# Kernel optimization log

Hardware: AMD Instinct MI355X
Metric: run time of the kernel (lower is better)

The kernel has to match this reference:

```python
import jax, jax.numpy as jnp
import numpy as np

V, E, H, L, B, T = 50257, 1024, 16, 8, 2, 2048
HD = E // H  # head_dim = 64
FF = 4 * E
EPS = 1e-5


def setup_inputs() -> dict:
    key = jax.random.key(0)
    ks = jax.random.split(key, 12)
    s = 0.02  # init std as in _init_weights
    return {
        "idx": jax.random.randint(ks[0], (B, T), 0, V, dtype=jnp.int64) if jax.config.jax_enable_x64 else jax.random.randint(ks[0], (B, T), 0, V, dtype=jnp.int32),
        "targets": jax.random.randint(ks[1], (B, T), 0, V, dtype=jnp.int32),
        "wte": jax.random.normal(ks[2], (V, E), jnp.float32) * s,
        "wpe": jax.random.normal(ks[3], (T, E), jnp.float32) * s,
        "qkv_w": jax.random.normal(ks[4], (L, E, 3 * E), jnp.float32) * s,
        "proj_w": jax.random.normal(ks[5], (L, E, E), jnp.float32) * s,
        "proj_b": jnp.zeros((L, E), jnp.float32),
        "ln1_g": jnp.ones((L, E), jnp.float32),
        "ln1_b": jnp.zeros((L, E), jnp.float32),
        "ln2_g": jnp.ones((L, E), jnp.float32),
        "ln2_b": jnp.zeros((L, E), jnp.float32),
        "fc1_w": jax.random.normal(ks[6], (L, E, FF), jnp.float32) * s,
        "fc1_b": jnp.zeros((L, FF), jnp.float32),
        "fc2_w": jax.random.normal(ks[7], (L, FF, E), jnp.float32) * s,
        "fc2_b": jnp.zeros((L, E), jnp.float32),
        "lnf_g": jnp.ones((E,), jnp.float32),
        "lnf_b": jnp.zeros((E,), jnp.float32),
    }


def _layer_norm(x, g, b):
    mean = x.mean(-1, keepdims=True)
    var = ((x - mean) ** 2).mean(-1, keepdims=True)  # unbiased=False
    return g * (x - mean) / jnp.sqrt(var + EPS) + b


def _gpt_forward(idx, targets, wte, wpe, qkv_w, proj_w, proj_b,
                 ln1_g, ln1_b, ln2_g, ln2_b, fc1_w, fc1_b, fc2_w, fc2_b,
                 lnf_g, lnf_b):
    Bq, Tq = idx.shape
    x = wte[idx] + wpe[:Tq][None, :, :]  # [B,T,E]
    causal = jnp.tril(jnp.ones((Tq, Tq), bool))  # [T,T]
    scale = 1.0 / np.sqrt(HD)

    def block(x, p):
        (qw, pw, pb, g1, b1, g2, b2, f1w, f1b, f2w, f2b) = p
        h = _layer_norm(x, g1, b1)
        qkv = h @ qw  # [B,T,3E]
        qkv = qkv.reshape(Bq, Tq, 3, H, HD).transpose(2, 0, 3, 1, 4)  # [3,B,H,T,HD]
        q, k, v = qkv[0], qkv[1], qkv[2]
        att = jnp.einsum('bhqd,bhkd->bhqk', q, k) * scale
        att = jnp.where(causal[None, None], att, -jnp.inf)
        att = jax.nn.softmax(att, axis=-1)  # dropout=0.0 -> identity
        y = jnp.einsum('bhqk,bhkd->bhqd', att, v)
        y = y.transpose(0, 2, 1, 3).reshape(Bq, Tq, E)
        x = x + y @ pw + pb
        h = _layer_norm(x, g2, b2)
        h = jax.nn.gelu(h @ f1w + f1b, approximate=False)  # torch nn.GELU = exact erf
        x = x + h @ f2w + f2b
        return x, None

    params = (qkv_w, proj_w, proj_b, ln1_g, ln1_b, ln2_g, ln2_b,
              fc1_w, fc1_b, fc2_w, fc2_b)
    x, _ = jax.lax.scan(block, x, params)
    x = _layer_norm(x, lnf_g, lnf_b)
    logits = x @ wte.T  # tied lm_head, [B,T,V]
    logp = jax.nn.log_softmax(logits, axis=-1)
    nll = -jnp.take_along_axis(logp, targets[..., None], axis=-1)[..., 0]
    loss = nll.mean()
    return logits, loss


def reference(idx, targets, wte, wpe, qkv_w, proj_w, proj_b,
              ln1_g, ln1_b, ln2_g, ln2_b, fc1_w, fc1_b, fc2_w, fc2_b,
              lnf_g, lnf_b):
    return _gpt_forward(idx, targets, wte, wpe, qkv_w, proj_w, proj_b,
                        ln1_g, ln1_b, ln2_g, ln2_b, fc1_w, fc1_b, fc2_w, fc2_b,
                        lnf_g, lnf_b)
```

## Files before the change

kernel.cpp:

```cpp
#include <hip/hip_runtime.h>
#include <math.h>

constexpr int Vv = 50257;
constexpr int Ee = 1024;
constexpr int Hh = 16;
constexpr int Ll = 8;
constexpr int Bb = 2;
constexpr int Tt = 2048;
constexpr int HDh = 64;
constexpr int FFf = 4096;
constexpr int BT = Bb * Tt;

typedef __attribute__((ext_vector_type(8))) short bf16x8;
typedef __attribute__((ext_vector_type(4))) float f32x4;

__device__ __forceinline__ short f2b(float f) {
    union { float f; unsigned u; } c; c.f = f;
    unsigned u = c.u + 0x7fffu + ((c.u >> 16) & 1u);
    return (short)(u >> 16);
}

__device__ __forceinline__ void g2l16(void* lds, const void* g) {
    __builtin_amdgcn_global_load_lds(
        (const __attribute__((address_space(1))) void*)g,
        (__attribute__((address_space(3))) void*)lds, 16, 0, 0);
}

__device__ __forceinline__ float gelu_exact(float v) {
    return 0.5f * v * (1.0f + erff(v * 0.70710678118654752f));
}

__global__ __launch_bounds__(256) void k_embed(const int* __restrict__ idx,
                                               const float* __restrict__ wte,
                                               const float* __restrict__ wpe,
                                               float* __restrict__ x) {
    const int row = blockIdx.x;
    const int t = row % Tt;
    const int tok = idx[row];
    const int c = threadIdx.x * 4;
    const float4 a = *(const float4*)(wte + (size_t)tok * Ee + c);
    const float4 b = *(const float4*)(wpe + (size_t)t * Ee + c);
    *(float4*)(x + (size_t)row * Ee + c) =
        make_float4(a.x + b.x, a.y + b.y, a.z + b.z, a.w + b.w);
}

__global__ __launch_bounds__(256) void k_ln(const float* __restrict__ x,
                                            const float* __restrict__ g,
                                            const float* __restrict__ b,
                                            short* __restrict__ out) {
    const int row = blockIdx.x;
    const int tid = threadIdx.x;
    const float4 v = *(const float4*)(x + (size_t)row * Ee + tid * 4);
    float s  = v.x + v.y + v.z + v.w;
    float ss = v.x * v.x + v.y * v.y + v.z * v.z + v.w * v.w;
#pragma unroll
    for (int off = 32; off; off >>= 1) {
        s  += __shfl_down(s, off);
        ss += __shfl_down(ss, off);
    }
    __shared__ float red[8];
    const int wid = tid >> 6, lane = tid & 63;
    if (lane == 0) { red[wid] = s; red[4 + wid] = ss; }
    __syncthreads();
    const float S  = red[0] + red[1] + red[2] + red[3];
    const float SS = red[4] + red[5] + red[6] + red[7];
    const float mean = S * (1.f / Ee);
    const float var  = SS * (1.f / Ee) - mean * mean;
    const float inv  = rsqrtf(var + 1e-5f);
    const float4 gg = *(const float4*)(g + tid * 4);
    const float4 bb = *(const float4*)(b + tid * 4);
    short4 o;
    o.x = f2b((v.x - mean) * inv * gg.x + bb.x);
    o.y = f2b((v.y - mean) * inv * gg.y + bb.y);
    o.z = f2b((v.z - mean) * inv * gg.z + bb.z);
    o.w = f2b((v.w - mean) * inv * gg.w + bb.w);
    *(short4*)(out + (size_t)row * Ee + tid * 4) = o;
}

__global__ __launch_bounds__(256) void k_wT(const float* __restrict__ w,
                                            short* __restrict__ o, int K, int N) {
    __shared__ short t[32][33];
    const int n0 = blockIdx.x * 32, k0 = blockIdx.y * 32;
    const int tid = threadIdx.x;
    {
        const int k = tid >> 3, n4 = (tid & 7) * 4;
        const float4 v = *(const float4*)(w + (size_t)(k0 + k) * N + n0 + n4);
        t[n4 + 0][k] = f2b(v.x); t[n4 + 1][k] = f2b(v.y);
        t[n4 + 2][k] = f2b(v.z); t[n4 + 3][k] = f2b(v.w);
    }
    __syncthreads();
    {
        const int n = tid >> 3, k4 = (tid & 7) * 4;
        short4 s;
        s.x = t[n][k4]; s.y = t[n][k4 + 1]; s.z = t[n][k4 + 2]; s.w = t[n][k4 + 3];
        *(short4*)(o + (size_t)(n0 + n) * K + k0 + k4) = s;
    }
}

__global__ __launch_bounds__(256) void k_vT(const short* __restrict__ qkv,
                                            short* __restrict__ vT) {
    __shared__ short t[32][33];
    const int r0 = blockIdx.x * 32;
    const int c0 = blockIdx.y * 32;
    const int tid = threadIdx.x;
    {
        const int r = tid >> 3, c4 = (tid & 7) * 4;
        const short4 v = *(const short4*)(qkv + (size_t)(r0 + r) * (3 * Ee) + 2 * Ee + c0 + c4);
        t[c4 + 0][r] = v.x; t[c4 + 1][r] = v.y;
        t[c4 + 2][r] = v.z; t[c4 + 3][r] = v.w;
    }
    __syncthreads();
    {
        const int c = tid >> 3, r4 = (tid & 7) * 4;
        short4 s;
        s.x = t[c][r4]; s.y = t[c][r4 + 1]; s.z = t[c][r4 + 2]; s.w = t[c][r4 + 3];
        *(short4*)(vT + (size_t)(c0 + c) * BT + r0 + r4) = s;
    }
}

__global__ __launch_bounds__(256) void k_cvt(const float* __restrict__ w,
                                             short* __restrict__ o, int n8) {
    const int i = blockIdx.x * 256 + threadIdx.x;
    if (i >= n8) return;
    const float4 a = ((const float4*)w)[i * 2];
    const float4 b = ((const float4*)w)[i * 2 + 1];
    bf16x8 v = {f2b(a.x), f2b(a.y), f2b(a.z), f2b(a.w),
                f2b(b.x), f2b(b.y), f2b(b.z), f2b(b.w)};
    ((bf16x8*)o)[i] = v;
}

__device__ __forceinline__ void st_c(float* C, size_t i, float v) { C[i] = v; }
__device__ __forceinline__ void st_c(short* C, size_t i, float v) { C[i] = f2b(v); }

template <int EPI, int SWZ, int BN64f, int WAVES, typename OT>
__global__ __launch_bounds__(WAVES * 64) void k_gemm(const short* __restrict__ A,
                                              const short* __restrict__ Bp,
                                              const float* __restrict__ bias,
                                              const float* __restrict__ res,
                                              OT* __restrict__ C,
                                              int M, int N, int K,
                                              float* __restrict__ pmax,
                                              float* __restrict__ psum) {
    constexpr int BM = (WAVES / 2) * 64;
    constexpr int BN = BN64f ? 64 : 128;
    constexpr int NJ = BN64f ? 2 : 4;
    constexpr int WCOL = BN64f ? 32 : 64;
    __shared__ short As[2][BM * 32];
    __shared__ short Bs[2][BN * 32];
    const int tid = threadIdx.x, w = tid >> 6, ln = tid & 63;
    int bx = blockIdx.x, by = blockIdx.y;
    if (SWZ) {
        const int nwg = gridDim.x * gridDim.y;
        const int orig = by * gridDim.x + bx;
        const int q = nwg >> 3, r = nwg & 7;
        const int xcd = orig & 7, local = orig >> 3;
        const int wgid = (xcd < r ? xcd * (q + 1) : r * (q + 1) + (xcd - r) * q) + local;
        if (SWZ == 1) { bx = wgid % gridDim.x; by = wgid / gridDim.x; }
        else          { bx = wgid / gridDim.y; by = wgid % gridDim.y; }
    }
    const int m0 = bx * BM, n0 = by * BN;
    const int wr = w >> 1, wc = w & 1;

    f32x4 zero = {0.f, 0.f, 0.f, 0.f};
    f32x4 acc[4][NJ];
#pragma unroll
    for (int i = 0; i < 4; i++)
#pragma unroll
        for (int j = 0; j < NJ; j++) acc[i][j] = zero;

    const int srow = w * 32 + (ln >> 2);
    const int scol = (ln & 3) * 8;
    const int sb   = tid >> 2;
    const int sb8  = w * 16 + (ln >> 2);
    const int br0 = min(n0 + srow, N - 1);
    const int br1 = min(n0 + srow + 16, N - 1);
    const int brs = min(n0 + sb, N - 1);
    const int br8 = min(n0 + sb8, N - 1);

    auto STAGE = [&](int buf, int k0) {
        short* As_ = As[buf];
        short* Bs_ = Bs[buf];
        g2l16(&As_[(w * 32 + 0) * 32],  A + (size_t)(m0 + srow) * K + k0 + scol);
        g2l16(&As_[(w * 32 + 16) * 32], A + (size_t)(m0 + srow + 16) * K + k0 + scol);
        if (BN64f) {
            g2l16(&Bs_[sb * 32], Bp + (size_t)brs * K + k0 + scol);
        } else if (WAVES == 8) {
            g2l16(&Bs_[(w * 16) * 32], Bp + (size_t)br8 * K + k0 + scol);
        } else {
            g2l16(&Bs_[(w * 32 + 0) * 32],  Bp + (size_t)br0 * K + k0 + scol);
            g2l16(&Bs_[(w * 32 + 16) * 32], Bp + (size_t)br1 * K + k0 + scol);
        }
    };

    int cur = 0;
    STAGE(0, 0);
    __syncthreads();
    for (int k0 = 0; k0 < K; k0 += 32) {
        if (k0 + 32 < K) STAGE(cur ^ 1, k0 + 32);
        const short* Ar = As[cur];
        const short* Br = Bs[cur];
        bf16x8 af[4], bfv[NJ];
#pragma unroll
        for (int i = 0; i < 4; i++)
            af[i]  = *(const bf16x8*)&Ar[(wr * 64 + i * 16 + (ln & 15)) * 32 + (ln >> 4) * 8];
#pragma unroll
        for (int j = 0; j < NJ; j++)
            bfv[j] = *(const bf16x8*)&Br[(wc * WCOL + j * 16 + (ln & 15)) * 32 + (ln >> 4) * 8];
#pragma unroll
        for (int i = 0; i < 4; i++)
#pragma unroll
            for (int j = 0; j < NJ; j++)
                acc[i][j] = __builtin_amdgcn_mfma_f32_16x16x32_bf16(
                    af[i], bfv[j], acc[i][j], 0, 0, 0);
        __syncthreads();
        cur ^= 1;
    }

#pragma unroll
    for (int j = 0; j < NJ; j++) {
        const int gcol = n0 + wc * WCOL + j * 16 + (ln & 15);
        if (gcol < N) {
            const float bv = (EPI == 2 || EPI == 3) ? bias[gcol] : 0.f;
#pragma unroll
            for (int i = 0; i < 4; i++) {
#pragma unroll
                for (int r = 0; r < 4; r++) {
                    const int grow = m0 + wr * 64 + i * 16 + (ln >> 4) * 4 + r;
                    float v = acc[i][j][r] + bv;
                    if (EPI == 2) v = gelu_exact(v);
                    if (EPI == 3) v += res[(size_t)grow * N + gcol];
                    st_c(C, (size_t)grow * N + gcol, v);
                }
            }
        }
    }
    if (EPI == 4) {
        const size_t slot = (size_t)(by * 2 + wc) * M;
#pragma unroll
        for (int i = 0; i < 4; i++) {
#pragma unroll
            for (int r = 0; r < 4; r++) {
                const int grow = m0 + wr * 64 + i * 16 + (ln >> 4) * 4 + r;
                float vv[NJ], pm = -INFINITY;
#pragma unroll
                for (int j = 0; j < NJ; j++) {
                    const int gcol = n0 + wc * WCOL + j * 16 + (ln & 15);
                    vv[j] = (gcol < N) ? acc[i][j][r] : -INFINITY;
                    pm = fmaxf(pm, vv[j]);
                }
#pragma unroll
                for (int off = 1; off < 16; off <<= 1) pm = fmaxf(pm, __shfl_xor(pm, off));
                float ps = 0.f;
#pragma unroll
                for (int j = 0; j < NJ; j++)
                    ps += (vv[j] > -INFINITY) ? __expf(vv[j] - pm) : 0.f;
#pragma unroll
                for (int off = 1; off < 16; off <<= 1) ps += __shfl_xor(ps, off);
                if ((ln & 15) == 0) {
                    pmax[slot + grow] = pm;
                    psum[slot + grow] = ps;
                }
            }
        }
    }
}

__global__ __launch_bounds__(256) void k_attn(const short* __restrict__ qkv,
                                              const short* __restrict__ vT,
                                              short* __restrict__ y) {
    __shared__ short Kl[64][72];
    __shared__ short Vt[64][72];
    __shared__ short Pl[4][16][72];
    const int tid = threadIdx.x, w = tid >> 6, ln = tid & 63;
    const int lo = blockIdx.x;
    const int hi = (Tt / 64 - 1) - lo;
    const int h = blockIdx.y, b = blockIdx.z;
    const size_t base = ((size_t)b * Tt) * (3 * Ee) + h * HDh;
    const int q0s[2] = {lo * 64, hi * 64};

    bf16x8 qf[2][2];
#pragma unroll
    for (int s = 0; s < 2; s++) {
        const int qr = q0s[s] + w * 16 + (ln & 15);
        const short* qp = qkv + base + (size_t)qr * (3 * Ee) + (ln >> 4) * 8;
        qf[s][0] = *(const bf16x8*)(qp);
        qf[s][1] = *(const bf16x8*)(qp + 32);
    }

    f32x4 zero = {0.f, 0.f, 0.f, 0.f};
    f32x4 oc[2][4];
#pragma unroll
    for (int s = 0; s < 2; s++)
#pragma unroll
        for (int i = 0; i < 4; i++) oc[s][i] = zero;
    float mx[2][4], ls[2][4];
#pragma unroll
    for (int s = 0; s < 2; s++)
#pragma unroll
        for (int r = 0; r < 4; r++) { mx[s][r] = -INFINITY; ls[s][r] = 0.f; }

    const int nt = hi + 1;
    for (int j = 0; j < nt; j++) {
        const int kb = j * 64;
        __syncthreads();
        {
            const int r = tid >> 2, d0 = (tid & 3) * 16;
            const short* kp = qkv + base + Ee + (size_t)(kb + r) * (3 * Ee) + d0;
            *(bf16x8*)&Kl[r][d0]     = *(const bf16x8*)(kp);
            *(bf16x8*)&Kl[r][d0 + 8] = *(const bf16x8*)(kp + 8);
            const short* vp = vT + (size_t)(h * HDh + r) * BT + (size_t)b * Tt + kb + d0;
            *(bf16x8*)&Vt[r][d0]     = *(const bf16x8*)(vp);
            *(bf16x8*)&Vt[r][d0 + 8] = *(const bf16x8*)(vp + 8);
        }
        __syncthreads();

#pragma unroll
        for (int s = 1; s >= 0; s--) {
            if (s == 0 && j > lo) continue;
            f32x4 sc[4];
#pragma unroll
            for (int kcb = 0; kcb < 4; kcb++) {
                const int krow = kcb * 16 + (ln & 15);
                bf16x8 kf0 = *(bf16x8*)&Kl[krow][(ln >> 4) * 8];
                bf16x8 kf1 = *(bf16x8*)&Kl[krow][(ln >> 4) * 8 + 32];
                f32x4 ss = __builtin_amdgcn_mfma_f32_16x16x32_bf16(qf[s][0], kf0, zero, 0, 0, 0);
                sc[kcb]  = __builtin_amdgcn_mfma_f32_16x16x32_bf16(qf[s][1], kf1, ss, 0, 0, 0);
            }
            float pv[4][4];
            float tmv[4] = {-INFINITY, -INFINITY, -INFINITY, -INFINITY};
#pragma unroll
            for (int kcb = 0; kcb < 4; kcb++) {
                const int col = kb + kcb * 16 + (ln & 15);
#pragma unroll
                for (int r = 0; r < 4; r++) {
                    const int qr = q0s[s] + w * 16 + (ln >> 4) * 4 + r;
                    const float sv = (col <= qr) ? sc[kcb][r] * 0.125f : -INFINITY;
                    pv[kcb][r] = sv;
                    tmv[r] = fmaxf(tmv[r], sv);
                }
            }
#pragma unroll
            for (int off = 1; off < 16; off <<= 1)
#pragma unroll
                for (int r = 0; r < 4; r++) tmv[r] = fmaxf(tmv[r], __shfl_xor(tmv[r], off));
            float rs[4];
#pragma unroll
            for (int r = 0; r < 4; r++) {
                const float nm = fmaxf(mx[s][r], tmv[r]);
                const float alpha = __expf(mx[s][r] - nm);
                mx[s][r] = nm;
                float acc_s = 0.f;
#pragma unroll
                for (int kcb = 0; kcb < 4; kcb++) {
                    const float e = __expf(pv[kcb][r] - nm);
                    pv[kcb][r] = e;
                    acc_s += e;
                }
                rs[r] = acc_s;
                ls[s][r] *= alpha;
#pragma unroll
                for (int db = 0; db < 4; db++) oc[s][db][r] *= alpha;
            }
#pragma unroll
            for (int off = 1; off < 16; off <<= 1)
#pragma unroll
                for (int r = 0; r < 4; r++) rs[r] += __shfl_xor(rs[r], off);
#pragma unroll
            for (int r = 0; r < 4; r++) ls[s][r] += rs[r];
#pragma unroll
            for (int kcb = 0; kcb < 4; kcb++)
#pragma unroll
                for (int r = 0; r < 4; r++)
                    Pl[w][(ln >> 4) * 4 + r][kcb * 16 + (ln & 15)] = f2b(pv[kcb][r]);
            bf16x8 pf0 = *(bf16x8*)&Pl[w][ln & 15][(ln >> 4) * 8];
            bf16x8 pf1 = *(bf16x8*)&Pl[w][ln & 15][(ln >> 4) * 8 + 32];
#pragma unroll
            for (int db = 0; db < 4; db++) {
                const int drow = db * 16 + (ln & 15);
                bf16x8 vf0 = *(bf16x8*)&Vt[drow][(ln >> 4) * 8];
                bf16x8 vf1 = *(bf16x8*)&Vt[drow][(ln >> 4) * 8 + 32];
                oc[s][db] = __builtin_amdgcn_mfma_f32_16x16x32_bf16(pf0, vf0, oc[s][db], 0, 0, 0);
                oc[s][db] = __builtin_amdgcn_mfma_f32_16x16x32_bf16(pf1, vf1, oc[s][db], 0, 0, 0);
            }
        }
    }
#pragma unroll
    for (int s = 0; s < 2; s++)
#pragma unroll
        for (int r = 0; r < 4; r++) {
            const int qr = q0s[s] + w * 16 + (ln >> 4) * 4 + r;
            const float inv = 1.f / ls[s][r];
#pragma unroll
            for (int db = 0; db < 4; db++)
                y[(size_t)(b * Tt + qr) * Ee + h * HDh + db * 16 + (ln & 15)] =
                    f2b(oc[s][db][r] * inv);
        }
}

__global__ __launch_bounds__(256) void k_loss_fin(const float* __restrict__ pmax,
                                                  const float* __restrict__ psum,
                                                  const float* __restrict__ logits,
                                                  const int* __restrict__ targets,
                                                  float* __restrict__ rnll, int nt2) {
    const int row = blockIdx.x * 256 + threadIdx.x;
    float M = -INFINITY, S = 0.f;
    for (int i = 0; i < nt2; i++) {
        const float pm = pmax[(size_t)i * BT + row];
        const float ps = psum[(size_t)i * BT + row];
        const float nm = fmaxf(M, pm);
        S = S * __expf(M - nm) + ps * __expf(pm - nm);
        M = nm;
    }
    rnll[row] = (M + logf(S)) - logits[(size_t)row * Vv + targets[row]];
}

__global__ __launch_bounds__(256) void k_loss_final(const float* __restrict__ rnll,
                                                    float* __restrict__ loss) {
    const int tid = threadIdx.x;
    float s = 0.f;
    for (int i = tid; i < BT; i += 256) s += rnll[i];
#pragma unroll
    for (int off = 32; off; off >>= 1) s += __shfl_xor(s, off);
    __shared__ float red[4];
    if ((tid & 63) == 0) red[tid >> 6] = s;
    __syncthreads();
    if (tid == 0) loss[0] = (red[0] + red[1] + red[2] + red[3]) / (float)BT;
}

extern "C" void kernel_launch(void* const* d_in, const int* in_sizes, int n_in,
                              void* d_out, int out_size, void* d_ws, size_t ws_size,
                              hipStream_t stream) {
    const int*   idx     = (const int*)d_in[0];
    const int*   targets = (const int*)d_in[1];
    const float* wte     = (const float*)d_in[2];
    const float* wpe     = (const float*)d_in[3];
    const float* qkv_w   = (const float*)d_in[4];
    const float* proj_w  = (const float*)d_in[5];
    const float* proj_b  = (const float*)d_in[6];
    const float* ln1_g   = (const float*)d_in[7];
    const float* ln1_b   = (const float*)d_in[8];
    const float* ln2_g   = (const float*)d_in[9];
    const float* ln2_b   = (const float*)d_in[10];
    const float* fc1_w   = (const float*)d_in[11];
    const float* fc1_b   = (const float*)d_in[12];
    const float* fc2_w   = (const float*)d_in[13];
    const float* fc2_b   = (const float*)d_in[14];
    const float* lnf_g   = (const float*)d_in[15];
    const float* lnf_b   = (const float*)d_in[16];

    float* logits = (float*)d_out;
    float* loss   = logits + (size_t)BT * Vv;

    constexpr int NT2 = 2 * ((Vv + 127) / 128);

    short* wteb = (short*)d_ws;
    float* x    = (float*)d_ws;
    short* qkvb = (short*)(x + (size_t)BT * Ee);
    short* y    = qkvb + (size_t)BT * 3 * Ee;
    short* h1   = y + (size_t)BT * Ee;
    short* wT   = h1 + (size_t)BT * FFf;
    short* vT   = wT + (size_t)FFf * Ee;
    const size_t OFF = (size_t)Vv * Ee * 2;
    short* h    = (short*)((char*)d_ws + OFF);
    float* rnll = (float*)(h + (size_t)BT * Ee);
    float* pmax = rnll + BT;
    float* psum = pmax + (size_t)BT * NT2;
    const size_t need = OFF + (size_t)BT * Ee * 2
                      + (BT + 2 * (size_t)BT * NT2) * sizeof(float);
    if (ws_size < need) return;

    k_embed<<<BT, 256, 0, stream>>>(idx, wte, wpe, x);
    for (int l = 0; l < Ll; l++) {
        k_ln<<<BT, 256, 0, stream>>>(x, ln1_g + (size_t)l * Ee, ln1_b + (size_t)l * Ee, h);
        k_wT<<<dim3(3 * Ee / 32, Ee / 32), 256, 0, stream>>>(
            qkv_w + (size_t)l * Ee * 3 * Ee, wT, Ee, 3 * Ee);
        k_gemm<0, 1, 0, 8, short><<<dim3(BT / 256, 3 * Ee / 128), 512, 0, stream>>>(
            h, wT, nullptr, nullptr, qkvb, BT, 3 * Ee, Ee, nullptr, nullptr);
        k_vT<<<dim3(BT / 32, Ee / 32), 256, 0, stream>>>(qkvb, vT);
        k_attn<<<dim3(Tt / 128, Hh, Bb), 256, 0, stream>>>(qkvb, vT, y);
        k_wT<<<dim3(Ee / 32, Ee / 32), 256, 0, stream>>>(
            proj_w + (size_t)l * Ee * Ee, wT, Ee, Ee);
        k_gemm<3, 1, 1, 4, float><<<dim3(BT / 128, Ee / 64), 256, 0, stream>>>(
            y, wT, proj_b + (size_t)l * Ee, x, x, BT, Ee, Ee, nullptr, nullptr);
        k_ln<<<BT, 256, 0, stream>>>(x, ln2_g + (size_t)l * Ee, ln2_b + (size_t)l * Ee, h);
        k_wT<<<dim3(FFf / 32, Ee / 32), 256, 0, stream>>>(
            fc1_w + (size_t)l * Ee * FFf, wT, Ee, FFf);
        k_gemm<2, 1, 0, 8, short><<<dim3(BT / 256, FFf / 128), 512, 0, stream>>>(
            h, wT, fc1_b + (size_t)l * FFf, nullptr, h1, BT, FFf, Ee, nullptr, nullptr);
        k_wT<<<dim3(Ee / 32, FFf / 32), 256, 0, stream>>>(
            fc2_w + (size_t)l * FFf * Ee, wT, FFf, Ee);
        k_gemm<3, 1, 1, 4, float><<<dim3(BT / 128, Ee / 64), 256, 0, stream>>>(
            h1, wT, fc2_b + (size_t)l * Ee, x, x, BT, Ee, FFf, nullptr, nullptr);
    }
    k_ln<<<BT, 256, 0, stream>>>(x, lnf_g, lnf_b, h);
    k_cvt<<<(Vv * Ee / 8 + 255) / 256, 256, 0, stream>>>(wte, wteb, Vv * Ee / 8);
    k_gemm<4, 2, 0, 8, float><<<dim3(BT / 256, (Vv + 127) / 128), 512, 0, stream>>>(
        h, wteb, nullptr, nullptr, logits, BT, Vv, Ee, pmax, psum);
    k_loss_fin<<<BT / 256, 256, 0, stream>>>(pmax, psum, logits, targets, rnll, NT2);
    k_loss_final<<<1, 256, 0, stream>>>(rnll, loss);
}
```

Before: 3.478 ms.

## Fuse layernorm, weight transposes and V transpose into combined prep launches; double-buffer attention K/V

LayerNorm, weight transpose-conversion and V transpose are merged into one multi-role kernel dispatched by block index. This cuts the per-layer launch count and lets the independent pieces run concurrently; a second weight buffer lets fc1 and fc2 weights be prepared together, and vT now reuses the h1 buffer. The attention kernel double-buffers K/V tiles in shared memory, prefetching the next tile into registers while computing the current one, removing one barrier per iteration. The cost is more LDS per attention block and a reworked workspace layout.

Result: no change. 3.449 ms (median of 2 runs) (-0.9%).

```diff
diff --git a/kernel.cpp b/kernel.cpp
--- a/kernel.cpp
+++ b/kernel.cpp
@@ -77,44 +77,80 @@
     *(short4*)(out + (size_t)row * Ee + tid * 4) = o;
 }
 
-__global__ __launch_bounds__(256) void k_wT(const float* __restrict__ w,
-                                            short* __restrict__ o, int K, int N) {
-    __shared__ short t[32][33];
-    const int n0 = blockIdx.x * 32, k0 = blockIdx.y * 32;
-    const int tid = threadIdx.x;
+__global__ __launch_bounds__(256) void k_prep(
+    const float* __restrict__ x, const float* __restrict__ g,
+    const float* __restrict__ b, short* __restrict__ hout, int nln,
+    const float* __restrict__ w1, short* __restrict__ o1, int K1, int N1, int nw1,
+    const float* __restrict__ w2, short* __restrict__ o2, int K2, int N2, int nw2,
+    const short* __restrict__ qkvsrc, short* __restrict__ vTo, int nvt) {
+    __shared__ float red[8];
+    __shared__ short tl[32][33];
+    const int blk = blockIdx.x, tid = threadIdx.x;
+    if (blk < nln) {
+        const int row = blk;
+        const float4 v = *(const float4*)(x + (size_t)row * Ee + tid * 4);
+        float s  = v.x + v.y + v.z + v.w;
+        float ss = v.x * v.x + v.y * v.y + v.z * v.z + v.w * v.w;
+#pragma unroll
+        for (int off = 32; off; off >>= 1) {
+            s  += __shfl_down(s, off);
+            ss += __shfl_down(ss, off);
+        }
+        const int wid = tid >> 6, lane = tid & 63;
+        if (lane == 0) { red[wid] = s; red[4 + wid] = ss; }
+        __syncthreads();
+        const float S  = red[0] + red[1] + red[2] + red[3];
+        const float SS = red[4] + red[5] + red[6] + red[7];
+        const float mean = S * (1.f / Ee);
+        const float var  = SS * (1.f / Ee) - mean * mean;
+        const float inv  = rsqrtf(var + 1e-5f);
+        const float4 gg = *(const float4*)(g + tid * 4);
+        const float4 bb = *(const float4*)(b + tid * 4);
+        short4 o;
+        o.x = f2b((v.x - mean) * inv * gg.x + bb.x);
+        o.y = f2b((v.y - mean) * inv * gg.y + bb.y);
+        o.z = f2b((v.z - mean) * inv * gg.z + bb.z);
+        o.w = f2b((v.w - mean) * inv * gg.w + bb.w);
+        *(short4*)(hout + (size_t)row * Ee + tid * 4) = o;
+        return;
+    }
+    int t = blk - nln;
+    if (t >= nw1 + nw2) {
+        t -= nw1 + nw2;
+        const int rx = BT / 32;
+        const int r0 = (t % rx) * 32, c0 = (t / rx) * 32;
+        {
+            const int r = tid >> 3, c4 = (tid & 7) * 4;
+            const short4 v = *(const short4*)(qkvsrc + (size_t)(r0 + r) * (3 * Ee) + 2 * Ee + c0 + c4);
+            tl[c4 + 0][r] = v.x; tl[c4 + 1][r] = v.y;
+            tl[c4 + 2][r] = v.z; tl[c4 + 3][r] = v.w;
+        }
+        __syncthreads();
+        {
+            const int c = tid >> 3, r4 = (tid & 7) * 4;
+            short4 s;
+            s.x = tl[c][r4]; s.y = tl[c][r4 + 1]; s.z = tl[c][r4 + 2]; s.w = tl[c][r4 + 3];
+            *(short4*)(vTo + (size_t)(c0 + c) * BT + r0 + r4) = s;
+        }
+        return;
+    }
+    const float* w; short* o; int K, N;
+    if (t < nw1) { w = w1; o = o1; K = K1; N = N1; }
+    else         { t -= nw1; w = w2; o = o2; K = K2; N = N2; }
+    const int nx = N / 32;
+    const int n0 = (t % nx) * 32, k0 = (t / nx) * 32;
     {
         const int k = tid >> 3, n4 = (tid & 7) * 4;
         const float4 v = *(const float4*)(w + (size_t)(k0 + k) * N + n0 + n4);
-        t[n4 + 0][k] = f2b(v.x); t[n4 + 1][k] = f2b(v.y);
-        t[n4 + 2][k] = f2b(v.z); t[n4 + 3][k] = f2b(v.w);
+        tl[n4 + 0][k] = f2b(v.x); tl[n4 + 1][k] = f2b(v.y);
+        tl[n4 + 2][k] = f2b(v.z); tl[n4 + 3][k] = f2b(v.w);
     }
     __syncthreads();
     {
         const int n = tid >> 3, k4 = (tid & 7) * 4;
         short4 s;
-        s.x = t[n][k4]; s.y = t[n][k4 + 1]; s.z = t[n][k4 + 2]; s.w = t[n][k4 + 3];
+        s.x = tl[n][k4]; s.y = tl[n][k4 + 1]; s.z = tl[n][k4 + 2]; s.w = tl[n][k4 + 3];
         *(short4*)(o + (size_t)(n0 + n) * K + k0 + k4) = s;
-    }
-}
-
-__global__ __launch_bounds__(256) void k_vT(const short* __restrict__ qkv,
-                                            short* __restrict__ vT) {
-    __shared__ short t[32][33];
-    const int r0 = blockIdx.x * 32;
-    const int c0 = blockIdx.y * 32;
-    const int tid = threadIdx.x;
-    {
-        const int r = tid >> 3, c4 = (tid & 7) * 4;
-        const short4 v = *(const short4*)(qkv + (size_t)(r0 + r) * (3 * Ee) + 2 * Ee + c0 + c4);
-        t[c4 + 0][r] = v.x; t[c4 + 1][r] = v.y;
-        t[c4 + 2][r] = v.z; t[c4 + 3][r] = v.w;
-    }
-    __syncthreads();
-    {
-        const int c = tid >> 3, r4 = (tid & 7) * 4;
-        short4 s;
-        s.x = t[c][r4]; s.y = t[c][r4 + 1]; s.z = t[c][r4 + 2]; s.w = t[c][r4 + 3];
-        *(short4*)(vT + (size_t)(c0 + c) * BT + r0 + r4) = s;
     }
 }
 
@@ -268,8 +304,8 @@
 __global__ __launch_bounds__(256) void k_attn(const short* __restrict__ qkv,
                                               const short* __restrict__ vT,
                                               short* __restrict__ y) {
-    __shared__ short Kl[64][72];
-    __shared__ short Vt[64][72];
+    __shared__ short Kl[2][64][72];
+    __shared__ short Vt[2][64][72];
     __shared__ short Pl[4][16][72];
     const int tid = threadIdx.x, w = tid >> 6, ln = tid & 63;
     const int lo = blockIdx.x;
@@ -277,6 +313,7 @@
     const int h = blockIdx.y, b = blockIdx.z;
     const size_t base = ((size_t)b * Tt) * (3 * Ee) + h * HDh;
     const int q0s[2] = {lo * 64, hi * 64};
+    const int sr = tid >> 2, sd0 = (tid & 3) * 16;
 
     bf16x8 qf[2][2];
 #pragma unroll
@@ -299,21 +336,31 @@
 #pragma unroll
         for (int r = 0; r < 4; r++) { mx[s][r] = -INFINITY; ls[s][r] = 0.f; }
 
+    bf16x8 kr0, kr1, vr0, vr1;
+    auto LOAD = [&](int j) {
+        const int kb = j * 64;
+        const short* kp = qkv + base + Ee + (size_t)(kb + sr) * (3 * Ee) + sd0;
+        kr0 = *(const bf16x8*)(kp);
+        kr1 = *(const bf16x8*)(kp + 8);
+        const short* vp = vT + (size_t)(h * HDh + sr) * BT + (size_t)b * Tt + kb + sd0;
+        vr0 = *(const bf16x8*)(vp);
+        vr1 = *(const bf16x8*)(vp + 8);
+    };
+    auto WRITE = [&](int buf) {
+        *(bf16x8*)&Kl[buf][sr][sd0]     = kr0;
+        *(bf16x8*)&Kl[buf][sr][sd0 + 8] = kr1;
+        *(bf16x8*)&Vt[buf][sr][sd0]     = vr0;
+        *(bf16x8*)&Vt[buf][sr][sd0 + 8] = vr1;
+    };
+
     const int nt = hi + 1;
+    LOAD(0); WRITE(0);
+    __syncthreads();
+    int cur = 0;
     for (int j = 0; j < nt; j++) {
         const int kb = j * 64;
-        __syncthreads();
-        {
-            const int r = tid >> 2, d0 = (tid & 3) * 16;
-            const short* kp = qkv + base + Ee + (size_t)(kb + r) * (3 * Ee) + d0;
-            *(bf16x8*)&Kl[r][d0]     = *(const bf16x8*)(kp);
-            *(bf16x8*)&Kl[r][d0 + 8] = *(const bf16x8*)(kp + 8);
-            const short* vp = vT + (size_t)(h * HDh + r) * BT + (size_t)b * Tt + kb + d0;
-            *(bf16x8*)&Vt[r][d0]     = *(const bf16x8*)(vp);
-            *(bf16x8*)&Vt[r][d0 + 8] = *(const bf16x8*)(vp + 8);
-        }
-        __syncthreads();
-
+        const bool pf = (j + 1 < nt);
+        if (pf) LOAD(j + 1);
 #pragma unroll
         for (int s = 1; s >= 0; s--) {
             if (s == 0 && j > lo) continue;
@@ -321,8 +368,8 @@
 #pragma unroll
             for (int kcb = 0; kcb < 4; kcb++) {
                 const int krow = kcb * 16 + (ln & 15);
-                bf16x8 kf0 = *(bf16x8*)&Kl[krow][(ln >> 4) * 8];
-                bf16x8 kf1 = *(bf16x8*)&Kl[krow][(ln >> 4) * 8 + 32];
+                bf16x8 kf0 = *(bf16x8*)&Kl[cur][krow][(ln >> 4) * 8];
+                bf16x8 kf1 = *(bf16x8*)&Kl[cur][krow][(ln >> 4) * 8 + 32];
                 f32x4 ss = __builtin_amdgcn_mfma_f32_16x16x32_bf16(qf[s][0], kf0, zero, 0, 0, 0);
                 sc[kcb]  = __builtin_amdgcn_mfma_f32_16x16x32_bf16(qf[s][1], kf1, ss, 0, 0, 0);
             }
@@ -377,12 +424,15 @@
 #pragma unroll
             for (int db = 0; db < 4; db++) {
                 const int drow = db * 16 + (ln & 15);
-                bf16x8 vf0 = *(bf16x8*)&Vt[drow][(ln >> 4) * 8];
-                bf16x8 vf1 = *(bf16x8*)&Vt[drow][(ln >> 4) * 8 + 32];
+                bf16x8 vf0 = *(bf16x8*)&Vt[cur][drow][(ln >> 4) * 8];
+                bf16x8 vf1 = *(bf16x8*)&Vt[cur][drow][(ln >> 4) * 8 + 32];
                 oc[s][db] = __builtin_amdgcn_mfma_f32_16x16x32_bf16(pf0, vf0, oc[s][db], 0, 0, 0);
                 oc[s][db] = __builtin_amdgcn_mfma_f32_16x16x32_bf16(pf1, vf1, oc[s][db], 0, 0, 0);
             }
         }
+        if (pf) WRITE(cur ^ 1);
+        __syncthreads();
+        cur ^= 1;
     }
 #pragma unroll
     for (int s = 0; s < 2; s++)
@@ -459,8 +509,12 @@
     short* y    = qkvb + (size_t)BT * 3 * Ee;
     short* h1   = y + (size_t)BT * Ee;
     short* wT   = h1 + (size_t)BT * FFf;
-    short* vT   = wT + (size_t)FFf * Ee;
-    const size_t OFF = (size_t)Vv * Ee * 2;
+    short* wT2  = wT + (size_t)FFf * Ee;
+    short* vT   = h1;
+    const size_t LAYER_END = ((size_t)BT * Ee * 4)
+                           + ((size_t)BT * (3 * Ee + Ee + FFf) + 2 * (size_t)FFf * Ee) * 2;
+    const size_t OFF0 = (size_t)Vv * Ee * 2;
+    const size_t OFF = (LAYER_END > OFF0 ? LAYER_END : OFF0 + 255) & ~(size_t)255;
     short* h    = (short*)((char*)d_ws + OFF);
     float* rnll = (float*)(h + (size_t)BT * Ee);
     float* pmax = rnll + BT;
@@ -471,26 +525,30 @@
 
     k_embed<<<BT, 256, 0, stream>>>(idx, wte, wpe, x);
     for (int l = 0; l < Ll; l++) {
-        k_ln<<<BT, 256, 0, stream>>>(x, ln1_g + (size_t)l * Ee, ln1_b + (size_t)l * Ee, h);
-        k_wT<<<dim3(3 * Ee / 32, Ee / 32), 256, 0, stream>>>(
-            qkv_w + (size_t)l * Ee * 3 * Ee, wT, Ee, 3 * Ee);
+        k_prep<<<4096 + 3072, 256, 0, stream>>>(
+            x, ln1_g + (size_t)l * Ee, ln1_b + (size_t)l * Ee, h, 4096,
+            qkv_w + (size_t)l * Ee * 3 * Ee, wT, Ee, 3 * Ee, 3072,
+            nullptr, nullptr, 0, 0, 0,
+            nullptr, nullptr, 0);
         k_gemm<0, 1, 0, 8, short><<<dim3(BT / 256, 3 * Ee / 128), 512, 0, stream>>>(
             h, wT, nullptr, nullptr, qkvb, BT, 3 * Ee, Ee, nullptr, nullptr);
-        k_vT<<<dim3(BT / 32, Ee / 32), 256, 0, stream>>>(qkvb, vT);
+        k_prep<<<1024 + 4096, 256, 0, stream>>>(
+            x, lnf_g, lnf_b, h, 0,
+            proj_w + (size_t)l * Ee * Ee, wT2, Ee, Ee, 1024,
+            nullptr, nullptr, 0, 0, 0,
+            qkvb, vT, 4096);
         k_attn<<<dim3(Tt / 128, Hh, Bb), 256, 0, stream>>>(qkvb, vT, y);
-        k_wT<<<dim3(Ee / 32, Ee / 32), 256, 0, stream>>>(
-            proj_w + (size_t)l * Ee * Ee, wT, Ee, Ee);
         k_gemm<3, 1, 1, 4, float><<<dim3(BT / 128, Ee / 64), 256, 0, stream>>>(
-            y, wT, proj_b + (size_t)l * Ee, x, x, BT, Ee, Ee, nullptr, nullptr);
-        k_ln<<<BT, 256, 0, stream>>>(x, ln2_g + (size_t)l * Ee, ln2_b + (size_t)l * Ee, h);
-        k_wT<<<dim3(FFf / 32, Ee / 32), 256, 0, stream>>>(
-            fc1_w + (size_t)l * Ee * FFf, wT, Ee, FFf);
+            y, wT2, proj_b + (size_t)l * Ee, x, x, BT, Ee, Ee, nullptr, nullptr);
+        k_prep<<<4096 + 4096 + 4096, 256, 0, stream>>>(
+            x, ln2_g + (size_t)l * Ee, ln2_b + (size_t)l * Ee, h, 4096,
+            fc1_w + (size_t)l * Ee * FFf, wT, Ee, FFf, 4096,
+            fc2_w + (size_t)l * FFf * Ee, wT2, FFf, Ee, 4096,
+            nullptr, nullptr, 0);
         k_gemm<2, 1, 0, 8, short><<<dim3(BT / 256, FFf / 128), 512, 0, stream>>>(
             h, wT, fc1_b + (size_t)l * FFf, nullptr, h1, BT, FFf, Ee, nullptr, nullptr);
-        k_wT<<<dim3(Ee / 32, FFf / 32), 256, 0, stream>>>(
-            fc2_w + (size_t)l * FFf * Ee, wT, FFf, Ee);
         k_gemm<3, 1, 1, 4, float><<<dim3(BT / 128, Ee / 64), 256, 0, stream>>>(
-            h1, wT, fc2_b + (size_t)l * Ee, x, x, BT, Ee, FFf, nullptr, nullptr);
+            h1, wT2, fc2_b + (size_t)l * Ee, x, x, BT, Ee, FFf, nullptr, nullptr);
     }
     k_ln<<<BT, 256, 0, stream>>>(x, lnf_g, lnf_b, h);
     k_cvt<<<(Vv * Ee / 8 + 255) / 256, 256, 0, stream>>>(wte, wteb, Vv * Ee / 8);
```
